# Performance work log

Hardware: AMD Instinct MI355X
Metric: run time of the kernel (lower is better)

## Reference

```python
import jax, jax.numpy as jnp
import numpy as np

DN = ('NCHW', 'OIHW', 'NCHW')

def conv(x, w, b, s, p):
    y = jax.lax.conv_general_dilated(x, w, (s, s), [(p, p), (p, p)], dimension_numbers=DN)
    return y if b is None else y + b[None, :, None, None]

def convT(x, w, b, s, p):
    # w is torch ConvTranspose2d layout (I, O, k, k); flip spatial, swap I/O
    k = w.shape[2]
    wf = jnp.flip(w, (2, 3)).transpose(1, 0, 2, 3)
    pad = k - 1 - p
    y = jax.lax.conv_general_dilated(x, wf, (1, 1), [(pad, pad), (pad, pad)],
                                     lhs_dilation=(s, s), dimension_numbers=DN)
    return y + b[None, :, None, None]

def res_stack(x, layers):
    # each layer: ReLU -> 3x3 conv (no bias) -> ReLU -> 1x1 conv (no bias), residual add
    for wa, wb in layers:
        x = x + conv(jax.nn.relu(conv(jax.nn.relu(x), wa, None, 1, 1)), wb, None, 1, 0)
    return jax.nn.relu(x)

def setup_inputs() -> dict:
    key = jax.random.key(0)
    ks = jax.random.split(key, 24)
    g = lambda i, shp: jax.random.normal(ks[i], shp, jnp.float32) * 0.05
    D, K = 64, 1024
    return {
        'patch': jax.random.normal(ks[0], (64, 3, 128, 128), jnp.float32),
        # encoder
        'ew1': g(1, (64, 3, 4, 4)),    'eb1': g(2, (64,)),
        'ew2': g(3, (128, 64, 4, 4)),  'eb2': g(4, (128,)),
        'ew3': g(5, (128, 128, 3, 3)), 'eb3': g(6, (128,)),
        'er1a': g(7, (32, 128, 3, 3)), 'er1b': g(8, (128, 32, 1, 1)),
        'er2a': g(9, (32, 128, 3, 3)), 'er2b': g(10, (128, 32, 1, 1)),
        # pre-quantization 1x1 conv
        'pqw': g(11, (D, 128, 1, 1)),  'pqb': g(12, (D,)),
        # codebook
        'emb': g(13, (K, D)) * 20.0,
        # decoder (ConvTranspose weights in torch (I,O,k,k) layout)
        'dw1': g(14, (D, 128, 3, 3)),  'db1': g(15, (128,)),
        'dr1a': g(16, (32, 128, 3, 3)), 'dr1b': g(17, (128, 32, 1, 1)),
        'dr2a': g(18, (32, 128, 3, 3)), 'dr2b': g(19, (128, 32, 1, 1)),
        'dw2': g(20, (128, 64, 4, 4)), 'db2': g(21, (64,)),
        'dw3': g(22, (64, 3, 4, 4)),   'db3': g(23, (3,)),
    }

def reference(patch, ew1, eb1, ew2, eb2, ew3, eb3, er1a, er1b, er2a, er2b,
              pqw, pqb, emb, dw1, db1, dr1a, dr1b, dr2a, dr2b, dw2, db2, dw3, db3):
    # encoder: 3x128x128 -> 128x32x32
    h = jax.nn.relu(conv(patch, ew1, eb1, 2, 1))
    h = jax.nn.relu(conv(h, ew2, eb2, 2, 1))
    h = conv(h, ew3, eb3, 1, 1)
    h = res_stack(h, [(er1a, er1b), (er2a, er2b)])
    z = conv(h, pqw, pqb, 1, 0)                      # [B, D, 32, 32]
    z = z.transpose(0, 2, 3, 1)                      # [B, 32, 32, D]
    B, H, W, D = z.shape
    zf = z.reshape(-1, D)                            # [N, D]
    # squared L2 distances to codebook, argmin
    dists = (jnp.sum(zf * zf, axis=1, keepdims=True)
             + jnp.sum(emb * emb, axis=1)
             - 2.0 * zf @ emb.T)                     # [N, K]
    idx = jnp.argmin(dists, axis=1)                  # [N]
    z_q = emb[idx].reshape(B, H, W, D)               # gather == one-hot matmul
    commitment_loss = jnp.mean((jax.lax.stop_gradient(z_q) - z) ** 2)
    codebook_loss = jnp.mean((z_q - jax.lax.stop_gradient(z)) ** 2)
    z_q = z + jax.lax.stop_gradient(z_q - z)         # straight-through
    z_q = z_q.transpose(0, 3, 1, 2)                  # [B, D, 32, 32]
    # decoder: D x 32x32 -> 3x128x128
    d = convT(z_q, dw1, db1, 1, 1)
    d = res_stack(d, [(dr1a, dr1b), (dr2a, dr2b)])
    d = jax.nn.relu(convT(d, dw2, db2, 2, 1))
    recon = convT(d, dw3, db3, 2, 1)
    return recon, codebook_loss, commitment_loss, idx[:, None]
```

## Files before the change

### kernel.cpp

```cpp
#include <hip/hip_runtime.h>
#include <hip/hip_bf16.h>

typedef __hip_bfloat16 bf16;
typedef unsigned short u16;

#define R_RECON 3145728
#define N_IDX   65536

__device__ __forceinline__ float ldg_in(const void* p, int i, int fl) {
  return fl ? ((const float*)p)[i] : __bfloat162float(((const bf16*)p)[i]);
}
__device__ __forceinline__ float cvt(float v) { return v; }
__device__ __forceinline__ float cvt(bf16 v) { return __bfloat162float(v); }

__global__ __launch_bounds__(256) void k_detect(const u16* __restrict__ p, int* __restrict__ flag) {
  __shared__ int s;
  if (threadIdx.x == 0) s = 0;
  __syncthreads();
  for (int i = threadIdx.x; i < 4096; i += 256) {
    float f = __uint_as_float(((unsigned)p[i]) << 16);
    if (!(fabsf(f) < 16384.f)) atomicOr(&s, 1);
  }
  __syncthreads();
  if (threadIdx.x == 0) flag[0] = s;
}

template<typename T>
__device__ __forceinline__ void enc1_loop(
    const T* __restrict__ ip, int iy0, int cx0, const float* sW,
    float& a0, float& a1, float& a2, float& a3,
    float& b0, float& b1, float& b2, float& b3)
{
  #pragma unroll
  for (int ci = 0; ci < 3; ++ci) {
    const T* cp = ip + ci * 16384;
    #pragma unroll
    for (int ky = 0; ky < 4; ++ky) {
      int iy = iy0 + ky;
      if ((unsigned)iy < 128u) {
        const T* rp = cp + iy * 128;
        float x0 = (cx0 >= 0) ? cvt(rp[cx0]) : 0.f;
        float x1 = cvt(rp[cx0 + 1]), x2 = cvt(rp[cx0 + 2]);
        float x3 = cvt(rp[cx0 + 3]), x4 = cvt(rp[cx0 + 4]);
        float x5 = cvt(rp[cx0 + 5]), x6 = cvt(rp[cx0 + 6]);
        float x7 = cvt(rp[cx0 + 7]), x8 = cvt(rp[cx0 + 8]);
        float x9 = (cx0 + 9 < 128) ? cvt(rp[cx0 + 9]) : 0.f;
        const float* WA = sW + ci * 16 + ky * 4;
        float wa0 = WA[0], wa1 = WA[1], wa2 = WA[2], wa3 = WA[3];
        a0 = fmaf(x0, wa0, fmaf(x1, wa1, fmaf(x2, wa2, fmaf(x3, wa3, a0))));
        a1 = fmaf(x2, wa0, fmaf(x3, wa1, fmaf(x4, wa2, fmaf(x5, wa3, a1))));
        a2 = fmaf(x4, wa0, fmaf(x5, wa1, fmaf(x6, wa2, fmaf(x7, wa3, a2))));
        a3 = fmaf(x6, wa0, fmaf(x7, wa1, fmaf(x8, wa2, fmaf(x9, wa3, a3))));
        const float* WB = WA + 48;
        float wb0 = WB[0], wb1 = WB[1], wb2 = WB[2], wb3 = WB[3];
        b0 = fmaf(x0, wb0, fmaf(x1, wb1, fmaf(x2, wb2, fmaf(x3, wb3, b0))));
        b1 = fmaf(x2, wb0, fmaf(x3, wb1, fmaf(x4, wb2, fmaf(x5, wb3, b1))));
        b2 = fmaf(x4, wb0, fmaf(x5, wb1, fmaf(x6, wb2, fmaf(x7, wb3, b2))));
        b3 = fmaf(x6, wb0, fmaf(x7, wb1, fmaf(x8, wb2, fmaf(x9, wb3, b3))));
      }
    }
  }
}

__global__ __launch_bounds__(256) void k_enc1(
    const void* __restrict__ patch, const void* __restrict__ w,
    const void* __restrict__ bias, float* __restrict__ out,
    const int* __restrict__ flag, int n0)
{
  __shared__ float sW[96];
  __shared__ float sB[2];
  int fl = flag[0];
  int bid = blockIdx.x;
  int rg = bid & 3; int t = bid >> 2;
  int cp = t & 31;  int n = t >> 5;
  int co0 = cp * 2;
  int tid = threadIdx.x;
  if (tid < 96) sW[tid] = ldg_in(w, co0 * 48 + tid, fl);
  if (tid < 2)  sB[tid] = ldg_in(bias, co0 + tid, fl);
  __syncthreads();
  int ty = tid >> 4, txq = tid & 15;
  int oy = rg * 16 + ty;
  int ox0 = txq * 4;
  int iy0 = 2 * oy - 1, cx0 = 2 * ox0 - 1;
  float bv0 = sB[0], bv1 = sB[1];
  float a0 = bv0, a1 = bv0, a2 = bv0, a3 = bv0;
  float b0 = bv1, b1 = bv1, b2 = bv1, b3 = bv1;
  size_t ibase = (size_t)(n0 + n) * 49152;
  if (fl) enc1_loop((const float*)patch + ibase, iy0, cx0, sW, a0, a1, a2, a3, b0, b1, b2, b3);
  else    enc1_loop((const bf16*)patch + ibase, iy0, cx0, sW, a0, a1, a2, a3, b0, b1, b2, b3);
  float* op = out + (size_t)(n * 64 + co0) * 4096 + oy * 64 + ox0;
  op[0] = fmaxf(a0, 0.f); op[1] = fmaxf(a1, 0.f);
  op[2] = fmaxf(a2, 0.f); op[3] = fmaxf(a3, 0.f);
  op += 4096;
  op[0] = fmaxf(b0, 0.f); op[1] = fmaxf(b1, 0.f);
  op[2] = fmaxf(b2, 0.f); op[3] = fmaxf(b3, 0.f);
}

#define E2_CO(PX, CL) { \
  float4 wv = *(const float4*)(sWc + (CL) * 16 + ky * 4); \
  PX##0 = fmaf(x0, wv.x, fmaf(x1, wv.y, fmaf(x2, wv.z, fmaf(x3, wv.w, PX##0)))); \
  PX##1 = fmaf(x2, wv.x, fmaf(x3, wv.y, fmaf(x4, wv.z, fmaf(x5, wv.w, PX##1)))); \
  PX##2 = fmaf(x4, wv.x, fmaf(x5, wv.y, fmaf(x6, wv.z, fmaf(x7, wv.w, PX##2)))); \
  PX##3 = fmaf(x6, wv.x, fmaf(x7, wv.y, fmaf(x8, wv.z, fmaf(x9, wv.w, PX##3)))); }

#define E2_ST(PX, OP) \
  (OP)[0] = fmaxf(PX##0, 0.f); (OP)[1] = fmaxf(PX##1, 0.f); \
  (OP)[2] = fmaxf(PX##2, 0.f); (OP)[3] = fmaxf(PX##3, 0.f);

__global__ __launch_bounds__(256) void k_enc2(
    const float* __restrict__ in, const void* __restrict__ w,
    const void* __restrict__ bias, float* __restrict__ out,
    const int* __restrict__ flag)
{
  const int Cin = 64, Cout = 128;
  const int P = 65;
  __shared__ float sIn[64 * P + 2];
  __shared__ __align__(16) float sWc[128];
  int fl = flag[0];
  int bid = blockIdx.x;
  int cp = bid & 15, n = bid >> 4;
  int co0 = cp * 8;
  int tid = threadIdx.x;
  int oy = tid >> 3, ox0 = (tid & 7) << 2;
  float A0,A1,A2,A3, B0,B1,B2,B3, C0,C1,C2,C3, D0,D1,D2,D3;
  float E0,E1,E2,E3, F0,F1,F2,F3, G0,G1,G2,G3, H0,H1,H2,H3;
  {
    float bv;
    bv = ldg_in(bias, co0 + 0, fl); A0=bv; A1=bv; A2=bv; A3=bv;
    bv = ldg_in(bias, co0 + 1, fl); B0=bv; B1=bv; B2=bv; B3=bv;
    bv = ldg_in(bias, co0 + 2, fl); C0=bv; C1=bv; C2=bv; C3=bv;
    bv = ldg_in(bias, co0 + 3, fl); D0=bv; D1=bv; D2=bv; D3=bv;
    bv = ldg_in(bias, co0 + 4, fl); E0=bv; E1=bv; E2=bv; E3=bv;
    bv = ldg_in(bias, co0 + 5, fl); F0=bv; F1=bv; F2=bv; F3=bv;
    bv = ldg_in(bias, co0 + 6, fl); G0=bv; G1=bv; G2=bv; G3=bv;
    bv = ldg_in(bias, co0 + 7, fl); H0=bv; H1=bv; H2=bv; H3=bv;
  }
  int ry0 = 2 * oy - 1;
  int cx0 = 2 * ox0 - 1;
  const float* ip = in + (size_t)n * Cin * 4096;
  for (int ci = 0; ci < Cin; ++ci) {
    __syncthreads();
    {
      const float4* g4 = (const float4*)(ip + ci * 4096);
      #pragma unroll
      for (int j = 0; j < 4; ++j) {
        int i4 = tid + j * 256;
        float4 v = g4[i4];
        int flat = i4 * 4;
        int iy = flat >> 6, ix = flat & 63;
        float* dst = sIn + iy * P + ((iy >> 3) & 1) + ix;
        dst[0] = v.x; dst[1] = v.y; dst[2] = v.z; dst[3] = v.w;
      }
      if (tid < 32) {
        int cl = tid >> 2, k4 = (tid & 3) * 4;
        int src = (co0 + cl) * 1024 + ci * 16 + k4;
        sWc[cl * 16 + k4 + 0] = ldg_in(w, src + 0, fl);
        sWc[cl * 16 + k4 + 1] = ldg_in(w, src + 1, fl);
        sWc[cl * 16 + k4 + 2] = ldg_in(w, src + 2, fl);
        sWc[cl * 16 + k4 + 3] = ldg_in(w, src + 3, fl);
      }
    }
    __syncthreads();
    #pragma unroll
    for (int ky = 0; ky < 4; ++ky) {
      int iy = ry0 + ky;
      if ((unsigned)iy < 64u) {
        const float* rp = sIn + iy * P + ((iy >> 3) & 1);
        float x0 = (cx0 >= 0) ? rp[cx0] : 0.f;
        float x1 = rp[cx0 + 1], x2 = rp[cx0 + 2], x3 = rp[cx0 + 3], x4 = rp[cx0 + 4];
        float x5 = rp[cx0 + 5], x6 = rp[cx0 + 6], x7 = rp[cx0 + 7], x8 = rp[cx0 + 8];
        float x9 = (cx0 + 9 < 64) ? rp[cx0 + 9] : 0.f;
        E2_CO(A, 0) E2_CO(B, 1) E2_CO(C, 2) E2_CO(D, 3)
        E2_CO(E, 4) E2_CO(F, 5) E2_CO(G, 6) E2_CO(H, 7)
      }
    }
  }
  float* op = out + (size_t)(n * Cout + co0) * 1024 + oy * 32 + ox0;
  E2_ST(A, op) op += 1024;
  E2_ST(B, op) op += 1024;
  E2_ST(C, op) op += 1024;
  E2_ST(D, op) op += 1024;
  E2_ST(E, op) op += 1024;
  E2_ST(F, op) op += 1024;
  E2_ST(G, op) op += 1024;
  E2_ST(H, op)
}

#define LOAD10(RP) \
  x0 = (ox0 > 0) ? (RP)[ox0 - 1] : 0.f; \
  x1 = (RP)[ox0];     x2 = (RP)[ox0 + 1]; x3 = (RP)[ox0 + 2]; x4 = (RP)[ox0 + 3]; \
  x5 = (RP)[ox0 + 4]; x6 = (RP)[ox0 + 5]; x7 = (RP)[ox0 + 6]; x8 = (RP)[ox0 + 7]; \
  x9 = (ox0 < 24) ? (RP)[ox0 + 8] : 0.f; \
  if (IN_RELU) { \
    x0 = fmaxf(x0, 0.f); x1 = fmaxf(x1, 0.f); x2 = fmaxf(x2, 0.f); x3 = fmaxf(x3, 0.f); \
    x4 = fmaxf(x4, 0.f); x5 = fmaxf(x5, 0.f); x6 = fmaxf(x6, 0.f); x7 = fmaxf(x7, 0.f); \
    x8 = fmaxf(x8, 0.f); x9 = fmaxf(x9, 0.f); \
  }

#define C8(PX, W0, W1, W2) \
  PX##0 = fmaf(x0, W0, fmaf(x1, W1, fmaf(x2, W2, PX##0))); \
  PX##1 = fmaf(x1, W0, fmaf(x2, W1, fmaf(x3, W2, PX##1))); \
  PX##2 = fmaf(x2, W0, fmaf(x3, W1, fmaf(x4, W2, PX##2))); \
  PX##3 = fmaf(x3, W0, fmaf(x4, W1, fmaf(x5, W2, PX##3))); \
  PX##4 = fmaf(x4, W0, fmaf(x5, W1, fmaf(x6, W2, PX##4))); \
  PX##5 = fmaf(x5, W0, fmaf(x6, W1, fmaf(x7, W2, PX##5))); \
  PX##6 = fmaf(x6, W0, fmaf(x7, W1, fmaf(x8, W2, PX##6))); \
  PX##7 = fmaf(x7, W0, fmaf(x8, W1, fmaf(x9, W2, PX##7)));

#define ROW8_AB(KY) \
  C8(A, wa[3*KY], wa[3*KY+1], wa[3*KY+2]) \
  C8(B, wb[3*KY], wb[3*KY+1], wb[3*KY+2])

template<bool IN_RELU, bool TRANS_W, bool OUT_RELU, bool HAS_BIAS>
__global__ __launch_bounds__(256) void k_conv3x3_v4(
    const float* __restrict__ in, const void* __restrict__ w,
    const void* __restrict__ bias, float* __restrict__ out,
    const int* __restrict__ flag, int Cin, int Cout)
{
  const int HW = 1024;
  const int PP = 33;
  const int PLANE = 32 * PP;
  __shared__ float sW[4608];
  __shared__ float sIn[2 * 1056];
  int fl = flag[0];
  int nq = Cout >> 2;
  int bid = blockIdx.x;
  int qc = bid % nq, n = bid / nq;
  int co0 = qc * 4;
  int tid = threadIdx.x;
  int tot = 4 * Cin * 9;
  for (int i = tid; i < tot; i += 256) {
    int cl = i / (Cin * 9), rem = i % (Cin * 9);
    int ci = rem / 9, k = rem % 9;
    int src = TRANS_W ? ((ci * Cout + co0 + cl) * 9 + (8 - k))
                      : (((co0 + cl) * Cin + ci) * 9 + k);
    sW[i] = ldg_in(w, src, fl);
  }
  int cp = tid >> 7;
  int tt = tid & 127;
  int ty = tt >> 2;
  int tx = tt & 3;
  int ox0 = tx * 8;
  int coA = co0 + cp * 2;
  const float* WA = sW + (cp * 2) * Cin * 9;
  const float* WB = WA + Cin * 9;
  float bvA = HAS_BIAS ? ldg_in(bias, coA, fl) : 0.f;
  float bvB = HAS_BIAS ? ldg_in(bias, coA + 1, fl) : 0.f;
  float A0=bvA,A1=bvA,A2=bvA,A3=bvA,A4=bvA,A5=bvA,A6=bvA,A7=bvA;
  float B0=bvB,B1=bvB,B2=bvB,B3=bvB,B4=bvB,B5=bvB,B6=bvB,B7=bvB;
  const float* ip = in + (size_t)n * Cin * HW;
  for (int cb = 0; cb < Cin; cb += 2) {
    __syncthreads();
    {
      const float4* g4 = (const float4*)(ip + cb * HW);
      #pragma unroll
      for (int j = 0; j < 2; ++j) {
        int i4 = tid + j * 256;
        float4 v = g4[i4];
        int flat = i4 * 4;
        int pl = flat >> 10, rem = flat & 1023;
        float* dst = sIn + pl * PLANE + (rem >> 5) * PP + (rem & 31);
        dst[0] = v.x; dst[1] = v.y; dst[2] = v.z; dst[3] = v.w;
      }
    }
    __syncthreads();
    #pragma unroll
    for (int u = 0; u < 2; ++u) {
      int ci = cb + u;
      const float* sP = sIn + u * PLANE;
      const float* wa = WA + ci * 9;
      const float* wb = WB + ci * 9;
      float x0, x1, x2, x3, x4, x5, x6, x7, x8, x9;
      if (ty > 0) {
        LOAD10(sP + (ty - 1) * PP)
        ROW8_AB(0)
      }
      {
        LOAD10(sP + ty * PP)
        ROW8_AB(1)
      }
      if (ty < 31) {
        LOAD10(sP + (ty + 1) * PP)
        ROW8_AB(2)
      }
    }
  }
  float* op = out + (size_t)(n * Cout + coA) * HW + ty * 32 + ox0;
  if (OUT_RELU) {
    op[0] = fmaxf(A0, 0.f); op[1] = fmaxf(A1, 0.f); op[2] = fmaxf(A2, 0.f); op[3] = fmaxf(A3, 0.f);
    op[4] = fmaxf(A4, 0.f); op[5] = fmaxf(A5, 0.f); op[6] = fmaxf(A6, 0.f); op[7] = fmaxf(A7, 0.f);
    op += HW;
    op[0] = fmaxf(B0, 0.f); op[1] = fmaxf(B1, 0.f); op[2] = fmaxf(B2, 0.f); op[3] = fmaxf(B3, 0.f);
    op[4] = fmaxf(B4, 0.f); op[5] = fmaxf(B5, 0.f); op[6] = fmaxf(B6, 0.f); op[7] = fmaxf(B7, 0.f);
  } else {
    op[0] = A0; op[1] = A1; op[2] = A2; op[3] = A3;
    op[4] = A4; op[5] = A5; op[6] = A6; op[7] = A7;
    op += HW;
    op[0] = B0; op[1] = B1; op[2] = B2; op[3] = B3;
    op[4] = B4; op[5] = B5; op[6] = B6; op[7] = B7;
  }
}

template<bool ACCUM, bool HAS_BIAS, bool OUT_RELU>
__global__ __launch_bounds__(256) void k_conv1x1_t4(
    const float* __restrict__ in, const void* __restrict__ w,
    const void* __restrict__ bias, float* __restrict__ out,
    const int* __restrict__ flag, int Cin, int Cout)
{
  const int HW = 1024;
  __shared__ float sW[512];
  int fl = flag[0];
  int nq = Cout >> 2;
  int bid = blockIdx.x;
  int qc = bid % nq, n = bid / nq;
  int co0 = qc * 4;
  int tid = threadIdx.x;
  for (int i = tid; i < 4 * Cin; i += 256)
    sW[i] = ldg_in(w, co0 * Cin + i, fl);
  __syncthreads();
  float acc[4][4];
  #pragma unroll
  for (int c = 0; c < 4; ++c) {
    float bv = HAS_BIAS ? ldg_in(bias, co0 + c, fl) : 0.f;
    #pragma unroll
    for (int k = 0; k < 4; ++k) acc[c][k] = bv;
  }
  const float* ip = in + (size_t)n * Cin * HW + tid;
  for (int ci = 0; ci < Cin; ++ci) {
    const float* p = ip + ci * HW;
    float x0 = p[0], x1 = p[256], x2 = p[512], x3 = p[768];
    #pragma unroll
    for (int c = 0; c < 4; ++c) {
      float wv = sW[c * Cin + ci];
      acc[c][0] = fmaf(wv, x0, acc[c][0]);
      acc[c][1] = fmaf(wv, x1, acc[c][1]);
      acc[c][2] = fmaf(wv, x2, acc[c][2]);
      acc[c][3] = fmaf(wv, x3, acc[c][3]);
    }
  }
  #pragma unroll
  for (int c = 0; c < 4; ++c) {
    float* op = out + (size_t)(n * Cout + co0 + c) * HW + tid;
    #pragma unroll
    for (int k = 0; k < 4; ++k) {
      float v = acc[c][k];
      if (ACCUM) v += op[k * 256];
      if (OUT_RELU) v = fmaxf(v, 0.f);
      op[k * 256] = v;
    }
  }
}

#define LOADW16V(BASE) { \
  const float4* w4_ = (const float4*)(BASE); \
  float4 t0_ = w4_[0], t1_ = w4_[1], t2_ = w4_[2], t3_ = w4_[3]; \
  w00 = t0_.x; w01 = t0_.y; w02 = t0_.z; w03 = t0_.w; \
  w10 = t1_.x; w11 = t1_.y; w12 = t1_.z; w13 = t1_.w; \
  w20 = t2_.x; w21 = t2_.y; w22 = t2_.z; w23 = t2_.w; \
  w30 = t3_.x; w31 = t3_.y; w32 = t3_.z; w33 = t3_.w; }

#define CT_J(P00, P01, P10, P11, M0, M1, M2, C0, C1, C2, D0, D1, D2) \
  P00 = fmaf(w11, C1, fmaf(w13, C0, fmaf(w31, M1, fmaf(w33, M0, P00)))); \
  P01 = fmaf(w10, C2, fmaf(w12, C1, fmaf(w30, M2, fmaf(w32, M1, P01)))); \
  P10 = fmaf(w01, D1, fmaf(w03, D0, fmaf(w21, C1, fmaf(w23, C0, P10)))); \
  P11 = fmaf(w00, D2, fmaf(w02, D1, fmaf(w20, C2, fmaf(w22, C1, P11))));

#define DECL16(PX, BV) \
  float PX##A0=BV, PX##A1=BV, PX##A2=BV, PX##A3=BV, \
        PX##B0=BV, PX##B1=BV, PX##B2=BV, PX##B3=BV, \
        PX##C0=BV, PX##C1=BV, PX##C2=BV, PX##C3=BV, \
        PX##D0=BV, PX##D1=BV, PX##D2=BV, PX##D3=BV;

#define CT_CO(PX) \
  CT_J(PX##A0, PX##B0, PX##C0, PX##D0, m0, m1, m2, c0, c1, c2, d0, d1, d2) \
  CT_J(PX##A1, PX##B1, PX##C1, PX##D1, m1, m2, m3, c1, c2, c3, d1, d2, d3) \
  CT_J(PX##A2, PX##B2, PX##C2, PX##D2, m2, m3, m4, c2, c3, c4, d2, d3, d4) \
  CT_J(PX##A3, PX##B3, PX##C3, PX##D3, m3, m4, m5, c3, c4, c5, d3, d4, d5)

#define CT_STORE(PX, PTR, HO) \
  (PTR)[0] = fmaxf(PX##A0, 0.f); (PTR)[1] = fmaxf(PX##B0, 0.f); \
  (PTR)[2] = fmaxf(PX##A1, 0.f); (PTR)[3] = fmaxf(PX##B1, 0.f); \
  (PTR)[4] = fmaxf(PX##A2, 0.f); (PTR)[5] = fmaxf(PX##B2, 0.f); \
  (PTR)[6] = fmaxf(PX##A3, 0.f); (PTR)[7] = fmaxf(PX##B3, 0.f); \
  (PTR)[HO]     = fmaxf(PX##C0, 0.f); (PTR)[HO + 1] = fmaxf(PX##D0, 0.f); \
  (PTR)[HO + 2] = fmaxf(PX##C1, 0.f); (PTR)[HO + 3] = fmaxf(PX##D1, 0.f); \
  (PTR)[HO + 4] = fmaxf(PX##C2, 0.f); (PTR)[HO + 5] = fmaxf(PX##D2, 0.f); \
  (PTR)[HO + 6] = fmaxf(PX##C3, 0.f); (PTR)[HO + 7] = fmaxf(PX##D3, 0.f);

__global__ __launch_bounds__(256) void k_convT_up1(
    const float* __restrict__ in, const void* __restrict__ w,
    const void* __restrict__ bias, float* __restrict__ out,
    const int* __restrict__ flag)
{
  const int Cin = 128, Cout = 64;
  const int PP = 33;
  __shared__ __align__(16) float sW[8192];
  __shared__ float sIn[32 * PP];
  int fl = flag[0];
  int bid = blockIdx.x;
  int cp = bid & 15, n = bid >> 4;
  int co0 = cp * 4;
  int tid = threadIdx.x;
  for (int i = tid; i < 8192; i += 256) {
    int cl = i >> 11, rem = i & 2047;
    int ci = rem >> 4, k = rem & 15;
    sW[i] = ldg_in(w, (ci * Cout + co0 + cl) * 16 + k, fl);
  }
  int qa = tid >> 3;
  int qb0 = (tid & 7) * 4;
  float bv0 = ldg_in(bias, co0, fl), bv1 = ldg_in(bias, co0 + 1, fl);
  float bv2 = ldg_in(bias, co0 + 2, fl), bv3 = ldg_in(bias, co0 + 3, fl);
  DECL16(u, bv0) DECL16(v, bv1) DECL16(y, bv2) DECL16(z, bv3)
  const float* ip = in + (size_t)n * Cin * 1024;
  bool vm = qa >= 1, vd = qa + 1 < 32;
  bool vl = qb0 > 0, vr = qb0 < 28;
  for (int ci = 0; ci < Cin; ++ci) {
    __syncthreads();
    {
      float4 g = ((const float4*)(ip + ci * 1024))[tid];
      float* dst = sIn + (tid >> 3) * PP + (tid & 7) * 4;
      dst[0] = g.x; dst[1] = g.y; dst[2] = g.z; dst[3] = g.w;
    }
    __syncthreads();
    const float* rm = sIn + (qa - 1) * PP;
    const float* rc = sIn + qa * PP;
    const float* rd = sIn + (qa + 1) * PP;
    float m0 = (vm && vl) ? rm[qb0 - 1] : 0.f;
    float m1 = vm ? rm[qb0] : 0.f, m2 = vm ? rm[qb0 + 1] : 0.f;
    float m3 = vm ? rm[qb0 + 2] : 0.f, m4 = vm ? rm[qb0 + 3] : 0.f;
    float m5 = (vm && vr) ? rm[qb0 + 4] : 0.f;
    float c0 = vl ? rc[qb0 - 1] : 0.f;
    float c1 = rc[qb0], c2 = rc[qb0 + 1], c3 = rc[qb0 + 2], c4 = rc[qb0 + 3];
    float c5 = vr ? rc[qb0 + 4] : 0.f;
    float d0 = (vd && vl) ? rd[qb0 - 1] : 0.f;
    float d1 = vd ? rd[qb0] : 0.f, d2 = vd ? rd[qb0 + 1] : 0.f;
    float d3 = vd ? rd[qb0 + 2] : 0.f, d4 = vd ? rd[qb0 + 3] : 0.f;
    float d5 = (vd && vr) ? rd[qb0 + 4] : 0.f;
    float w00, w01, w02, w03, w10, w11, w12, w13, w20, w21, w22, w23, w30, w31, w32, w33;
    { LOADW16V(sW + ci * 16)        CT_CO(u) }
    { LOADW16V(sW + 2048 + ci * 16) CT_CO(v) }
    { LOADW16V(sW + 4096 + ci * 16) CT_CO(y) }
    { LOADW16V(sW + 6144 + ci * 16) CT_CO(z) }
  }
  float* op = out + ((size_t)(n * Cout + co0) * 64 + 2 * qa) * 64 + 2 * qb0;
  CT_STORE(u, op, 64) op += (size_t)64 * 64;
  CT_STORE(v, op, 64) op += (size_t)64 * 64;
  CT_STORE(y, op, 64) op += (size_t)64 * 64;
  CT_STORE(z, op, 64)
}

__global__ __launch_bounds__(256) void k_convT_up2(
    const float* __restrict__ in, const void* __restrict__ w,
    const void* __restrict__ bias, float* __restrict__ out,
    const int* __restrict__ flag)
{
  const int Cin = 64;
  __shared__ __align__(16) float sW[3072];
  int fl = flag[0];
  int bid = blockIdx.x;
  int s = bid & 7, n = bid >> 3;
  int tid = threadIdx.x;
  for (int i = tid; i < 3072; i += 256)
    sW[i] = ldg_in(w, i, fl);
  __syncthreads();
  int qa = s * 8 + (tid >> 5);
  int qb0 = (tid & 31) * 2;
  float bp = ldg_in(bias, 0, fl), bq = ldg_in(bias, 1, fl), br = ldg_in(bias, 2, fl);
  float pA0 = bp, pA1 = bp, pB0 = bp, pB1 = bp, pC0 = bp, pC1 = bp, pD0 = bp, pD1 = bp;
  float qA0 = bq, qA1 = bq, qB0_ = bq, qB1 = bq, qC0 = bq, qC1 = bq, qD0 = bq, qD1 = bq;
  float rA0 = br, rA1 = br, rB0 = br, rB1 = br, rC0 = br, rC1 = br, rD0 = br, rD1 = br;
  const float* ip = in + (size_t)n * Cin * 4096;
  bool vm = qa >= 1, vd = qa + 1 < 64;
  bool vl = qb0 > 0, vr = qb0 < 62;
  for (int ci = 0; ci < Cin; ++ci) {
    const float* p = ip + ci * 4096;
    const float* rm = p + (qa - 1) * 64;
    const float* rc = p + qa * 64;
    const float* rd = p + (qa + 1) * 64;
    float m0 = (vm && vl) ? rm[qb0 - 1] : 0.f;
    float m1 = vm ? rm[qb0] : 0.f, m2 = vm ? rm[qb0 + 1] : 0.f;
    float m3 = (vm && vr) ? rm[qb0 + 2] : 0.f;
    float c0 = vl ? rc[qb0 - 1] : 0.f;
    float c1 = rc[qb0], c2 = rc[qb0 + 1];
    float c3 = vr ? rc[qb0 + 2] : 0.f;
    float d0 = (vd && vl) ? rd[qb0 - 1] : 0.f;
    float d1 = vd ? rd[qb0] : 0.f, d2 = vd ? rd[qb0 + 1] : 0.f;
    float d3 = (vd && vr) ? rd[qb0 + 2] : 0.f;
    float w00, w01, w02, w03, w10, w11, w12, w13, w20, w21, w22, w23, w30, w31, w32, w33;
    {
      LOADW16V(sW + ci * 48)
      CT_J(pA0, pB0, pC0, pD0, m0, m1, m2, c0, c1, c2, d0, d1, d2)
      CT_J(pA1, pB1, pC1, pD1, m1, m2, m3, c1, c2, c3, d1, d2, d3)
    }
    {
      LOADW16V(sW + ci * 48 + 16)
      CT_J(qA0, qB0_, qC0, qD0, m0, m1, m2, c0, c1, c2, d0, d1, d2)
      CT_J(qA1, qB1, qC1, qD1, m1, m2, m3, c1, c2, c3, d1, d2, d3)
    }
    {
      LOADW16V(sW + ci * 48 + 32)
      CT_J(rA0, rB0, rC0, rD0, m0, m1, m2, c0, c1, c2, d0, d1, d2)
      CT_J(rA1, rB1, rC1, rD1, m1, m2, m3, c1, c2, c3, d1, d2, d3)
    }
  }
  float* op = out + ((size_t)(n * 3 + 0) * 128 + 2 * qa) * 128 + 2 * qb0;
  op[0] = pA0; op[1] = pB0; op[2] = pA1; op[3] = pB1;
  op[128] = pC0; op[129] = pD0; op[130] = pC1; op[131] = pD1;
  op += (size_t)128 * 128;
  op[0] = qA0; op[1] = qB0_; op[2] = qA1; op[3] = qB1;
  op[128] = qC0; op[129] = qD0; op[130] = qC1; op[131] = qD1;
  op += (size_t)128 * 128;
  op[0] = rA0; op[1] = rB0; op[2] = rA1; op[3] = rB1;
  op[128] = rC0; op[129] = rD0; op[130] = rC1; op[131] = rD1;
}

__global__ __launch_bounds__(256) void k_vq1(
    const float* __restrict__ z, const void* __restrict__ emb,
    const int* __restrict__ flag, float* __restrict__ distb, float* __restrict__ idxb)
{
  const int PE = 68;
  __shared__ __align__(16) float sE[128 * PE];
  __shared__ float sEE[128];
  int fl = flag[0];
  int tid = threadIdx.x;
  int bid = blockIdx.x;
  int ch = bid & 3, vb = bid >> 2;
  int n = vb * 256 + tid;
  int nb = n >> 10, p = n & 1023;
  const float* zp = z + nb * 65536 + p;
  float zv[64];
  float zz = 0.f;
  #pragma unroll
  for (int d = 0; d < 64; ++d) { zv[d] = zp[d * 1024]; zz = fmaf(zv[d], zv[d], zz); }
  float best = 3.4e38f; int bidx = ch * 256;
  for (int kb = ch * 2; kb < ch * 2 + 2; ++kb) {
    __syncthreads();
    for (int i = tid; i < 8192; i += 256)
      sE[(i >> 6) * PE + (i & 63)] = ldg_in(emb, kb * 8192 + i, fl);
    __syncthreads();
    if (tid < 128) {
      const float4* ep4 = (const float4*)(sE + tid * PE);
      float s = 0.f;
      #pragma unroll
      for (int i = 0; i < 16; ++i) {
        float4 v = ep4[i];
        s = fmaf(v.x, v.x, s); s = fmaf(v.y, v.y, s);
        s = fmaf(v.z, v.z, s); s = fmaf(v.w, v.w, s);
      }
      sEE[tid] = s;
    }
    __syncthreads();
    #pragma unroll 2
    for (int k = 0; k < 128; ++k) {
      const float4* ep4 = (const float4*)(sE + k * PE);
      float dot = 0.f;
      #pragma unroll
      for (int i = 0; i < 16; ++i) {
        float4 v = ep4[i];
        dot = fmaf(zv[4*i],     v.x, dot);
        dot = fmaf(zv[4*i + 1], v.y, dot);
        dot = fmaf(zv[4*i + 2], v.z, dot);
        dot = fmaf(zv[4*i + 3], v.w, dot);
      }
      float dist = zz + sEE[k] - 2.f * dot;
      if (dist < best) { best = dist; bidx = kb * 128 + k; }
    }
  }
  distb[ch * 65536 + n] = best;
  idxb[ch * 65536 + n] = (float)bidx;
}

__global__ __launch_bounds__(256) void k_vq2(
    const float* __restrict__ z, const void* __restrict__ emb,
    const int* __restrict__ flag, const float* __restrict__ distb,
    const float* __restrict__ idxb, float* __restrict__ zq,
    float* __restrict__ idx_out, float* __restrict__ lossp, int lossbase)
{
  __shared__ float wsum[4];
  int fl = flag[0];
  int tid = threadIdx.x;
  int n = blockIdx.x * 256 + tid;
  float best = distb[n];
  int bidx = (int)idxb[n];
  #pragma unroll
  for (int c = 1; c < 4; ++c) {
    float d = distb[c * 65536 + n];
    if (d < best) { best = d; bidx = (int)idxb[c * 65536 + n]; }
  }
  idx_out[n] = (float)bidx;
  int nb = n >> 10, p = n & 1023;
  const float* zp = z + nb * 65536 + p;
  float* qp = zq + nb * 65536 + p;
  float ls = 0.f;
  #pragma unroll
  for (int d = 0; d < 64; ++d) {
    float e = ldg_in(emb, bidx * 64 + d, fl);
    float zvd = zp[d * 1024];
    qp[d * 1024] = e;
    float df = e - zvd;
    ls = fmaf(df, df, ls);
  }
  #pragma unroll
  for (int off = 32; off > 0; off >>= 1) ls += __shfl_down(ls, off);
  if ((tid & 63) == 0) wsum[tid >> 6] = ls;
  __syncthreads();
  if (tid == 0) lossp[lossbase + blockIdx.x] = wsum[0] + wsum[1] + wsum[2] + wsum[3];
}

__global__ void k_loss_final(const float* __restrict__ lossp, float* __restrict__ out) {
  if (threadIdx.x == 0 && blockIdx.x == 0) {
    float s = 0.f;
    for (int i = 0; i < 256; ++i) s += lossp[i];
    float L = s * (1.f / 4194304.f);
    out[R_RECON + 0] = L;
    out[R_RECON + 1] = L;
  }
}

extern "C" void kernel_launch(void* const* d_in, const int* in_sizes, int n_in,
                              void* d_out, int out_size, void* d_ws, size_t ws_size,
                              hipStream_t stream)
{
  float* out = (float*)d_out;

  float* F = (float*)d_ws;
  float* LOSSP = F;
  int* FLAG = (int*)(F + 256);
  float* VQD = F + 272;
  float* VQI = VQD + 262144;
  float* A = VQI + 262144;

  int Bc = 64;
  while (Bc > 1 && 4ull * (272ull + 524288ull + (size_t)Bc * 393216ull) > ws_size) Bc >>= 1;
  float* H1 = A;
  float* H2 = A + (size_t)Bc * 262144;
  float* H3 = A;
  float* T  = A + (size_t)Bc * 131072;
  float* Z  = A + (size_t)Bc * 163840;
  float* D1 = H2;
  float* D2 = A;

  const void* patch = d_in[0];
  const void* ew1 = d_in[1];  const void* eb1 = d_in[2];
  const void* ew2 = d_in[3];  const void* eb2 = d_in[4];
  const void* ew3 = d_in[5];  const void* eb3 = d_in[6];
  const void* er1a = d_in[7]; const void* er1b = d_in[8];
  const void* er2a = d_in[9]; const void* er2b = d_in[10];
  const void* pqw = d_in[11]; const void* pqb = d_in[12];
  const void* emb = d_in[13];
  const void* dw1 = d_in[14]; const void* db1 = d_in[15];
  const void* dr1a = d_in[16]; const void* dr1b = d_in[17];
  const void* dr2a = d_in[18]; const void* dr2b = d_in[19];
  const void* dw2 = d_in[20]; const void* db2 = d_in[21];
  const void* dw3 = d_in[22]; const void* db3 = d_in[23];

  k_detect<<<1, 256, 0, stream>>>((const u16*)patch, FLAG);

  int NC = 64 / Bc;
  for (int c = 0; c < NC; ++c) {
    int b0 = c * Bc;

    k_enc1<<<Bc * 128, 256, 0, stream>>>(patch, ew1, eb1, H1, FLAG, b0);
    k_enc2<<<Bc * 16, 256, 0, stream>>>(H1, ew2, eb2, H2, FLAG);
    k_conv3x3_v4<false, false, false, true><<<Bc * 32, 256, 0, stream>>>(H2, ew3, eb3, H3, FLAG, 128, 128);
    k_conv3x3_v4<true, false, true, false><<<Bc * 8, 256, 0, stream>>>(H3, er1a, nullptr, T, FLAG, 128, 32);
    k_conv1x1_t4<true, false, false><<<Bc * 32, 256, 0, stream>>>(T, er1b, nullptr, H3, FLAG, 32, 128);
    k_conv3x3_v4<true, false, true, false><<<Bc * 8, 256, 0, stream>>>(H3, er2a, nullptr, T, FLAG, 128, 32);
    k_conv1x1_t4<true, false, true><<<Bc * 32, 256, 0, stream>>>(T, er2b, nullptr, H3, FLAG, 32, 128);
    k_conv1x1_t4<false, true, false><<<Bc * 16, 256, 0, stream>>>(H3, pqw, pqb, Z, FLAG, 128, 64);

    k_vq1<<<Bc * 16, 256, 0, stream>>>(Z, emb, FLAG, VQD, VQI);
    k_vq2<<<Bc * 4, 256, 0, stream>>>(Z, emb, FLAG, VQD, VQI, Z,
                                      out + R_RECON + 2 + (size_t)b0 * 1024, LOSSP, b0 * 4);

    k_conv3x3_v4<false, true, false, true><<<Bc * 32, 256, 0, stream>>>(Z, dw1, db1, D1, FLAG, 64, 128);
    k_conv3x3_v4<true, false, true, false><<<Bc * 8, 256, 0, stream>>>(D1, dr1a, nullptr, T, FLAG, 128, 32);
    k_conv1x1_t4<true, false, false><<<Bc * 32, 256, 0, stream>>>(T, dr1b, nullptr, D1, FLAG, 32, 128);
    k_conv3x3_v4<true, false, true, false><<<Bc * 8, 256, 0, stream>>>(D1, dr2a, nullptr, T, FLAG, 128, 32);
    k_conv1x1_t4<true, false, true><<<Bc * 32, 256, 0, stream>>>(T, dr2b, nullptr, D1, FLAG, 32, 128);
    k_convT_up1<<<Bc * 16, 256, 0, stream>>>(D1, dw2, db2, D2, FLAG);
    k_convT_up2<<<Bc * 8, 256, 0, stream>>>(D2, dw3, db3, out + (size_t)b0 * 49152, FLAG);
  }

  k_loss_final<<<1, 64, 0, stream>>>(LOSSP, out);
}
```

Measured before the change: 1.951 ms.

## Compute four output channels per thread in 3x3 conv and stream weights per chunk

The 3x3 conv kernel now has each thread accumulate four output channels instead of two, so every block covers eight channels and half as many blocks are launched. Each input plane staged in shared memory is reused across twice as many channels, which halves redundant input loads. The full per-block weight preload into an 18KB shared array is replaced by a small 144-float buffer refilled each two-channel step, which cuts shared memory use. In exchange, register pressure rises (32 accumulators), there are fewer blocks to fill the GPU, and weight loads now sit inside the loop.

New measurement: 1.987 ms. No clear change (+1.8%).

```diff
diff --git a/kernel.cpp b/kernel.cpp
--- a/kernel.cpp
+++ b/kernel.cpp
@@ -207,12 +207,25 @@
   PX##6 = fmaf(x6, W0, fmaf(x7, W1, fmaf(x8, W2, PX##6))); \
   PX##7 = fmaf(x7, W0, fmaf(x8, W1, fmaf(x9, W2, PX##7)));
 
-#define ROW8_AB(KY) \
+#define ROW8_4(KY) \
   C8(A, wa[3*KY], wa[3*KY+1], wa[3*KY+2]) \
-  C8(B, wb[3*KY], wb[3*KY+1], wb[3*KY+2])
+  C8(B, wb[3*KY], wb[3*KY+1], wb[3*KY+2]) \
+  C8(C, wc[3*KY], wc[3*KY+1], wc[3*KY+2]) \
+  C8(D, wd[3*KY], wd[3*KY+1], wd[3*KY+2])
+
+#define ST8(PX, PTR) \
+  if (OUT_RELU) { \
+    (PTR)[0] = fmaxf(PX##0, 0.f); (PTR)[1] = fmaxf(PX##1, 0.f); \
+    (PTR)[2] = fmaxf(PX##2, 0.f); (PTR)[3] = fmaxf(PX##3, 0.f); \
+    (PTR)[4] = fmaxf(PX##4, 0.f); (PTR)[5] = fmaxf(PX##5, 0.f); \
+    (PTR)[6] = fmaxf(PX##6, 0.f); (PTR)[7] = fmaxf(PX##7, 0.f); \
+  } else { \
+    (PTR)[0] = PX##0; (PTR)[1] = PX##1; (PTR)[2] = PX##2; (PTR)[3] = PX##3; \
+    (PTR)[4] = PX##4; (PTR)[5] = PX##5; (PTR)[6] = PX##6; (PTR)[7] = PX##7; \
+  }
 
 template<bool IN_RELU, bool TRANS_W, bool OUT_RELU, bool HAS_BIAS>
-__global__ __launch_bounds__(256) void k_conv3x3_v4(
+__global__ __launch_bounds__(256) void k_conv3x3_v5(
     const float* __restrict__ in, const void* __restrict__ w,
     const void* __restrict__ bias, float* __restrict__ out,
     const int* __restrict__ flag, int Cin, int Cout)
@@ -220,34 +233,28 @@
   const int HW = 1024;
   const int PP = 33;
   const int PLANE = 32 * PP;
-  __shared__ float sW[4608];
   __shared__ float sIn[2 * 1056];
-  int fl = flag[0];
-  int nq = Cout >> 2;
+  __shared__ float sWc[144];
+  int fl = flag[0];
+  int nq = Cout >> 3;
   int bid = blockIdx.x;
   int qc = bid % nq, n = bid / nq;
-  int co0 = qc * 4;
-  int tid = threadIdx.x;
-  int tot = 4 * Cin * 9;
-  for (int i = tid; i < tot; i += 256) {
-    int cl = i / (Cin * 9), rem = i % (Cin * 9);
-    int ci = rem / 9, k = rem % 9;
-    int src = TRANS_W ? ((ci * Cout + co0 + cl) * 9 + (8 - k))
-                      : (((co0 + cl) * Cin + ci) * 9 + k);
-    sW[i] = ldg_in(w, src, fl);
-  }
-  int cp = tid >> 7;
+  int co0 = qc * 8;
+  int tid = threadIdx.x;
+  int half = tid >> 7;
   int tt = tid & 127;
   int ty = tt >> 2;
   int tx = tt & 3;
   int ox0 = tx * 8;
-  int coA = co0 + cp * 2;
-  const float* WA = sW + (cp * 2) * Cin * 9;
-  const float* WB = WA + Cin * 9;
+  int coA = co0 + half * 4;
   float bvA = HAS_BIAS ? ldg_in(bias, coA, fl) : 0.f;
   float bvB = HAS_BIAS ? ldg_in(bias, coA + 1, fl) : 0.f;
+  float bvC = HAS_BIAS ? ldg_in(bias, coA + 2, fl) : 0.f;
+  float bvD = HAS_BIAS ? ldg_in(bias, coA + 3, fl) : 0.f;
   float A0=bvA,A1=bvA,A2=bvA,A3=bvA,A4=bvA,A5=bvA,A6=bvA,A7=bvA;
   float B0=bvB,B1=bvB,B2=bvB,B3=bvB,B4=bvB,B5=bvB,B6=bvB,B7=bvB;
+  float C0=bvC,C1=bvC,C2=bvC,C3=bvC,C4=bvC,C5=bvC,C6=bvC,C7=bvC;
+  float D0=bvD,D1=bvD,D2=bvD,D3=bvD,D4=bvD,D5=bvD,D6=bvD,D7=bvD;
   const float* ip = in + (size_t)n * Cin * HW;
   for (int cb = 0; cb < Cin; cb += 2) {
     __syncthreads();
@@ -262,43 +269,44 @@
         float* dst = sIn + pl * PLANE + (rem >> 5) * PP + (rem & 31);
         dst[0] = v.x; dst[1] = v.y; dst[2] = v.z; dst[3] = v.w;
       }
+      if (tid < 144) {
+        int u = tid / 72, r = tid % 72;
+        int cl = r / 9, k = r % 9;
+        int ci = cb + u;
+        int src = TRANS_W ? ((ci * Cout + co0 + cl) * 9 + (8 - k))
+                          : (((co0 + cl) * Cin + ci) * 9 + k);
+        sWc[tid] = ldg_in(w, src, fl);
+      }
     }
     __syncthreads();
     #pragma unroll
     for (int u = 0; u < 2; ++u) {
-      int ci = cb + u;
       const float* sP = sIn + u * PLANE;
-      const float* wa = WA + ci * 9;
-      const float* wb = WB + ci * 9;
+      const float* wq = sWc + u * 72 + (half * 4) * 9;
+      const float* wa = wq;
+      const float* wb = wq + 9;
+      const float* wc = wq + 18;
+      const float* wd = wq + 27;
       float x0, x1, x2, x3, x4, x5, x6, x7, x8, x9;
       if (ty > 0) {
         LOAD10(sP + (ty - 1) * PP)
-        ROW8_AB(0)
+        ROW8_4(0)
       }
       {
         LOAD10(sP + ty * PP)
-        ROW8_AB(1)
+        ROW8_4(1)
       }
       if (ty < 31) {
         LOAD10(sP + (ty + 1) * PP)
-        ROW8_AB(2)
+        ROW8_4(2)
       }
     }
   }
   float* op = out + (size_t)(n * Cout + coA) * HW + ty * 32 + ox0;
-  if (OUT_RELU) {
-    op[0] = fmaxf(A0, 0.f); op[1] = fmaxf(A1, 0.f); op[2] = fmaxf(A2, 0.f); op[3] = fmaxf(A3, 0.f);
-    op[4] = fmaxf(A4, 0.f); op[5] = fmaxf(A5, 0.f); op[6] = fmaxf(A6, 0.f); op[7] = fmaxf(A7, 0.f);
-    op += HW;
-    op[0] = fmaxf(B0, 0.f); op[1] = fmaxf(B1, 0.f); op[2] = fmaxf(B2, 0.f); op[3] = fmaxf(B3, 0.f);
-    op[4] = fmaxf(B4, 0.f); op[5] = fmaxf(B5, 0.f); op[6] = fmaxf(B6, 0.f); op[7] = fmaxf(B7, 0.f);
-  } else {
-    op[0] = A0; op[1] = A1; op[2] = A2; op[3] = A3;
-    op[4] = A4; op[5] = A5; op[6] = A6; op[7] = A7;
-    op += HW;
-    op[0] = B0; op[1] = B1; op[2] = B2; op[3] = B3;
-    op[4] = B4; op[5] = B5; op[6] = B6; op[7] = B7;
-  }
+  ST8(A, op) op += HW;
+  ST8(B, op) op += HW;
+  ST8(C, op) op += HW;
+  ST8(D, op)
 }
 
 template<bool ACCUM, bool HAS_BIAS, bool OUT_RELU>
@@ -662,10 +670,10 @@
 
     k_enc1<<<Bc * 128, 256, 0, stream>>>(patch, ew1, eb1, H1, FLAG, b0);
     k_enc2<<<Bc * 16, 256, 0, stream>>>(H1, ew2, eb2, H2, FLAG);
-    k_conv3x3_v4<false, false, false, true><<<Bc * 32, 256, 0, stream>>>(H2, ew3, eb3, H3, FLAG, 128, 128);
-    k_conv3x3_v4<true, false, true, false><<<Bc * 8, 256, 0, stream>>>(H3, er1a, nullptr, T, FLAG, 128, 32);
+    k_conv3x3_v5<false, false, false, true><<<Bc * 16, 256, 0, stream>>>(H2, ew3, eb3, H3, FLAG, 128, 128);
+    k_conv3x3_v5<true, false, true, false><<<Bc * 4, 256, 0, stream>>>(H3, er1a, nullptr, T, FLAG, 128, 32);
     k_conv1x1_t4<true, false, false><<<Bc * 32, 256, 0, stream>>>(T, er1b, nullptr, H3, FLAG, 32, 128);
-    k_conv3x3_v4<true, false, true, false><<<Bc * 8, 256, 0, stream>>>(H3, er2a, nullptr, T, FLAG, 128, 32);
+    k_conv3x3_v5<true, false, true, false><<<Bc * 4, 256, 0, stream>>>(H3, er2a, nullptr, T, FLAG, 128, 32);
     k_conv1x1_t4<true, false, true><<<Bc * 32, 256, 0, stream>>>(T, er2b, nullptr, H3, FLAG, 32, 128);
     k_conv1x1_t4<false, true, false><<<Bc * 16, 256, 0, stream>>>(H3, pqw, pqb, Z, FLAG, 128, 64);
 
@@ -673,10 +681,10 @@
     k_vq2<<<Bc * 4, 256, 0, stream>>>(Z, emb, FLAG, VQD, VQI, Z,
                                       out + R_RECON + 2 + (size_t)b0 * 1024, LOSSP, b0 * 4);
 
-    k_conv3x3_v4<false, true, false, true><<<Bc * 32, 256, 0, stream>>>(Z, dw1, db1, D1, FLAG, 64, 128);
-    k_conv3x3_v4<true, false, true, false><<<Bc * 8, 256, 0, stream>>>(D1, dr1a, nullptr, T, FLAG, 128, 32);
+    k_conv3x3_v5<false, true, false, true><<<Bc * 16, 256, 0, stream>>>(Z, dw1, db1, D1, FLAG, 64, 128);
+    k_conv3x3_v5<true, false, true, false><<<Bc * 4, 256, 0, stream>>>(D1, dr1a, nullptr, T, FLAG, 128, 32);
     k_conv1x1_t4<true, false, false><<<Bc * 32, 256, 0, stream>>>(T, dr1b, nullptr, D1, FLAG, 32, 128);
-    k_conv3x3_v4<true, false, true, false><<<Bc * 8, 256, 0, stream>>>(D1, dr2a, nullptr, T, FLAG, 128, 32);
+    k_conv3x3_v5<true, false, true, false><<<Bc * 4, 256, 0, stream>>>(D1, dr2a, nullptr, T, FLAG, 128, 32);
     k_conv1x1_t4<true, false, true><<<Bc * 32, 256, 0, stream>>>(T, dr2b, nullptr, D1, FLAG, 32, 128);
     k_convT_up1<<<Bc * 16, 256, 0, stream>>>(D1, dw2, db2, D2, FLAG);
     k_convT_up2<<<Bc * 8, 256, 0, stream>>>(D2, dw3, db3, out + (size_t)b0 * 49152, FLAG);
```
